# Performance work log

Hardware: AMD Instinct MI355X
Metric: run time of the kernel (lower is better)

## Reference

```python
import jax, jax.numpy as jnp
import numpy as np

REGION_DIM = 144
LLM_DIM = 3584
NUM_HEADS = 4
HEAD_DIM = REGION_DIM // NUM_HEADS          # 36
V_HEAD_DIM = LLM_DIM // NUM_HEADS           # 896
LN_EPS = 1e-5
N, M = 4096, 4096


def setup_inputs() -> dict:
    key = jax.random.key(0)
    ks = jax.random.split(key, 16)
    s = 0.02
    return {
        "target_emb": jax.random.normal(ks[0], (N, REGION_DIM), jnp.float32),
        "source_emb": jax.random.normal(ks[1], (M, LLM_DIM), jnp.float32),
        "value_emb":  jax.random.normal(ks[2], (M, LLM_DIM), jnp.float32),
        # params stored [in, out] (transposed vs torch nn.Linear)
        "wq_w": jax.random.normal(ks[3], (REGION_DIM, REGION_DIM), jnp.float32) * s,
        "wq_b": jnp.zeros((REGION_DIM,), jnp.float32),
        "wk_w": jax.random.normal(ks[4], (LLM_DIM, REGION_DIM), jnp.float32) * s,
        "wk_b": jnp.zeros((REGION_DIM,), jnp.float32),
        # per-head V projections stacked: [H, llm_dim, llm_dim//H]
        "wv_w": jax.random.normal(ks[5], (NUM_HEADS, LLM_DIM, V_HEAD_DIM), jnp.float32) * s,
        "wv_b": jnp.zeros((NUM_HEADS, V_HEAD_DIM), jnp.float32),
        "resid_w": jax.random.normal(ks[6], (REGION_DIM, LLM_DIM), jnp.float32) * s,
        "resid_b": jnp.zeros((LLM_DIM,), jnp.float32),
        "out_w": jax.random.normal(ks[7], (LLM_DIM, LLM_DIM), jnp.float32) * s,
        "out_b": jnp.zeros((LLM_DIM,), jnp.float32),
        "ln_g": jnp.ones((LLM_DIM,), jnp.float32),
        "ln_b": jnp.zeros((LLM_DIM,), jnp.float32),
    }


def reference(target_emb, source_emb, value_emb,
              wq_w, wq_b, wk_w, wk_b, wv_w, wv_b,
              resid_w, resid_b, out_w, out_b, ln_g, ln_b):
    n = target_emb.shape[0]
    # Q: [N, region_dim] -> [H, N, head_dim]; K: [M, llm_dim] -> [H, M, head_dim]
    Q = (target_emb @ wq_w + wq_b).reshape(n, NUM_HEADS, HEAD_DIM).transpose(1, 0, 2)
    K = (source_emb @ wk_w + wk_b).reshape(-1, NUM_HEADS, HEAD_DIM).transpose(1, 0, 2)
    scores = jnp.einsum('hnd,hmd->hnm', Q, K) / jnp.sqrt(jnp.float32(HEAD_DIM))
    attn = jax.nn.softmax(scores, axis=-1)      # dropout = identity (eval mode)
    # per-head value projections: [H, M, llm_dim//H]
    V = jnp.einsum('me,hed->hmd', value_emb, wv_w) + wv_b[:, None, :]
    ctx = jnp.einsum('hnm,hmd->nhd', attn, V).reshape(n, LLM_DIM)
    x = ctx + (target_emb @ resid_w + resid_b)   # residual_proj (region_dim != llm_dim)
    mu = jnp.mean(x, axis=-1, keepdims=True)
    var = jnp.mean(jnp.square(x - mu), axis=-1, keepdims=True)
    x = (x - mu) * jax.lax.rsqrt(var + LN_EPS) * ln_g + ln_b
    return x @ out_w + out_b
```

## Files before the change

### kernel.cpp

```cpp
#include <hip/hip_runtime.h>

typedef _Float16 f16;
typedef _Float16 f16x8 __attribute__((ext_vector_type(8)));
typedef float f32x4 __attribute__((ext_vector_type(4)));

#define REGION_DIM 144
#define LLM_DIM 3584
#define NUM_HEADS 4
#define HEAD_DIM 36
#define HEAD_PAD 64
#define QK_COLS 256
#define KPAD_REGION 160
#define V_HEAD 896
#define LN_EPS 1e-5f

__device__ __forceinline__ void gl_lds16(const f16* g, f16* l)
{
    __builtin_amdgcn_global_load_lds(
        (const __attribute__((address_space(1))) unsigned int*)g,
        (__attribute__((address_space(3))) unsigned int*)l, 16, 0, 0);
}

__global__ void k_convert_pad(const float* __restrict__ in, f16* __restrict__ out,
                              int Cin, int Cout)
{
    int r = blockIdx.y;
    int c = blockIdx.x * 256 + threadIdx.x;
    if (c >= Cout) return;
    float v = (c < Cin) ? in[(long)r * Cin + c] : 0.f;
    out[(long)r * Cout + c] = (f16)v;
}

__global__ void k_transpose(const float* __restrict__ in, f16* __restrict__ out,
                            int R, int C, int Rpad, int Cpad,
                            long in_bstride, long out_bstride)
{
    __shared__ float tile[32][33];
    const float* ip = in + (long)blockIdx.z * in_bstride;
    f16* op = out + (long)blockIdx.z * out_bstride;
    int r0 = blockIdx.y * 32, c0 = blockIdx.x * 32;
    int tx = threadIdx.x, ty = threadIdx.y;
#pragma unroll
    for (int i = 0; i < 32; i += 8) {
        int r = r0 + ty + i, c = c0 + tx;
        tile[ty + i][tx] = (r < R && c < C) ? ip[(long)r * C + c] : 0.f;
    }
    __syncthreads();
#pragma unroll
    for (int i = 0; i < 32; i += 8) {
        int c = c0 + ty + i, r = r0 + tx;
        if (c < Cpad && r < Rpad) op[(long)c * Rpad + r] = (f16)tile[tx][ty + i];
    }
}

__global__ void k_headpad_w(const float* __restrict__ w, const float* __restrict__ b,
                            f16* __restrict__ outW, float* __restrict__ outB,
                            int E, int Epad)
{
    int hp = blockIdx.y;
    int h = hp >> 6, kk = hp & 63;
    int d = h * HEAD_DIM + kk;
    bool valid = (kk < HEAD_DIM);
    int e = blockIdx.x * 256 + threadIdx.x;
    if (e < Epad) {
        float v = (valid && e < E) ? w[(long)e * REGION_DIM + d] : 0.f;
        outW[(long)hp * Epad + e] = (f16)v;
    }
    if (blockIdx.x == 0 && threadIdx.x == 0) outB[hp] = valid ? b[d] : 0.f;
}

enum { EPI_F16_EXPSCALE = 0,
       EPI_F16_BIASROW  = 1,
       EPI_F16_DIVROW   = 2,
       EPI_F32_BIASCOL  = 3,
       EPI_F16_BIASCOL  = 4 };

template <int EPI>
__global__ __launch_bounds__(256, 2)
void gemm_f16(const f16* __restrict__ A, int lda, long sAz,
              const f16* __restrict__ Bt, int ldb, long sBz,
              void* __restrict__ Cv, int ldc, long sCz,
              const float* __restrict__ bias, long sbz, float scale, int K)
{
    __shared__ __align__(16) f16 sA[128 * 32];
    __shared__ __align__(16) f16 sB[128 * 32];
    const int tid = threadIdx.x;
    const int z = blockIdx.z;
    A += (long)z * sAz;
    Bt += (long)z * sBz;
    if (bias) bias += (long)z * sbz;

    const int gx = gridDim.x, gy = gridDim.y;
    int pid = blockIdx.y * gx + blockIdx.x;
    const int GROUP = 8;
    int span = GROUP * gx;
    int gid = pid / span;
    int y0 = gid * GROUP;
    int gsz = (gy - y0 < GROUP) ? (gy - y0) : GROUP;
    int rem = pid - gid * span;
    const int by = y0 + rem % gsz;
    const int bx = rem / gsz;
    const int m0 = by * 128, n0 = bx * 128;

    const int w = tid >> 6, l = tid & 63;
    const int wu = __builtin_amdgcn_readfirstlane(w);
    const int wr = w >> 1, wc = w & 1;

    f32x4 acc[4][4] = {};

    const int srow = tid >> 2;
    const int scol = (tid & 3) * 8;
    const f16* Ag = A + (long)(m0 + srow) * lda + scol;
    const f16* Bg = Bt + (long)(n0 + srow) * ldb + scol;
    f16* sA0 = sA + wu * 512;
    f16* sA1 = sA + 2048 + wu * 512;
    f16* sB0 = sB + wu * 512;
    f16* sB1 = sB + 2048 + wu * 512;
    const int qk = (l >> 4) * 8;
    const int fr = l & 15;

    for (int k0 = 0; k0 < K; k0 += 32) {
        __syncthreads();
        gl_lds16(Ag + k0, sA0);
        gl_lds16(Ag + (long)64 * lda + k0, sA1);
        gl_lds16(Bg + k0, sB0);
        gl_lds16(Bg + (long)64 * ldb + k0, sB1);
        __syncthreads();

        f16x8 af[4], bf[4];
#pragma unroll
        for (int mt = 0; mt < 4; mt++)
            af[mt] = *(const f16x8*)&sA[(wr * 64 + mt * 16 + fr) * 32 + qk];
#pragma unroll
        for (int nt = 0; nt < 4; nt++)
            bf[nt] = *(const f16x8*)&sB[(wc * 64 + nt * 16 + fr) * 32 + qk];
#pragma unroll
        for (int mt = 0; mt < 4; mt++)
#pragma unroll
            for (int nt = 0; nt < 4; nt++)
                acc[mt][nt] = __builtin_amdgcn_mfma_f32_16x16x32_f16(af[mt], bf[nt], acc[mt][nt], 0, 0, 0);
    }

    const int q4 = (l >> 4) * 4;
    float bc[4];
#pragma unroll
    for (int nt = 0; nt < 4; nt++) {
        if constexpr (EPI == EPI_F16_BIASCOL || EPI == EPI_F32_BIASCOL)
            bc[nt] = bias[n0 + wc * 64 + nt * 16 + fr];
        else
            bc[nt] = 0.f;
    }
#pragma unroll
    for (int mt = 0; mt < 4; mt++)
#pragma unroll
        for (int r = 0; r < 4; r++) {
            int row = m0 + wr * 64 + mt * 16 + q4 + r;
            float rowv = 0.f;
            if constexpr (EPI == EPI_F16_BIASROW) rowv = bias[row];
            if constexpr (EPI == EPI_F16_DIVROW) rowv = 1.f / bias[row];
#pragma unroll
            for (int nt = 0; nt < 4; nt++) {
                int col = n0 + wc * 64 + nt * 16 + fr;
                float v = acc[mt][nt][r];
                if constexpr (EPI == EPI_F16_EXPSCALE) {
                    ((f16*)Cv + (long)z * sCz)[(long)row * ldc + col] = (f16)__expf(v * scale);
                } else if constexpr (EPI == EPI_F16_BIASROW) {
                    ((f16*)Cv + (long)z * sCz)[(long)row * ldc + col] = (f16)(v + rowv);
                } else if constexpr (EPI == EPI_F16_DIVROW) {
                    ((f16*)Cv + (long)z * sCz)[(long)row * ldc + col] = (f16)(v * rowv);
                } else if constexpr (EPI == EPI_F16_BIASCOL) {
                    ((f16*)Cv + (long)z * sCz)[(long)row * ldc + col] = (f16)(v + bc[nt]);
                } else {
                    ((float*)Cv + (long)z * sCz)[(long)row * ldc + col] = v + bc[nt];
                }
            }
        }
}

__global__ void k_rowsum(const f16* __restrict__ P, float* __restrict__ lsum,
                         long hstride)
{
    const f16x8* p8 = (const f16x8*)(P + (long)blockIdx.y * hstride + (long)blockIdx.x * 4096);
    int t = threadIdx.x, w = t >> 6, l = t & 63;
    f16x8 a = p8[t], b = p8[256 + t];
    float s = 0.f;
#pragma unroll
    for (int j = 0; j < 8; j++) s += (float)a[j] + (float)b[j];
#pragma unroll
    for (int o = 32; o; o >>= 1) s += __shfl_xor(s, o);
    __shared__ float red[4];
    if (l == 0) red[w] = s;
    __syncthreads();
    if (t == 0)
        lsum[(long)blockIdx.y * gridDim.x + blockIdx.x] = red[0] + red[1] + red[2] + red[3];
}

__global__ void k_layernorm(const f16* __restrict__ ctxp, const f16* __restrict__ resp,
                            const float* __restrict__ g, const float* __restrict__ be,
                            f16* __restrict__ out)
{
    long base = (long)blockIdx.x * LLM_DIM;
    const f16x8* c8 = (const f16x8*)(ctxp + base);
    const f16x8* r8 = (const f16x8*)(resp + base);
    int t = threadIdx.x, w = t >> 6, l = t & 63;
    bool has2 = t < 192;
    f16x8 a0 = c8[t], b0 = r8[t];
    f16x8 a1 = {}, b1 = {};
    if (has2) { a1 = c8[256 + t]; b1 = r8[256 + t]; }
    float v[16];
    float s = 0.f;
#pragma unroll
    for (int j = 0; j < 8; j++) { v[j] = (float)a0[j] + (float)b0[j]; s += v[j]; }
#pragma unroll
    for (int j = 0; j < 8; j++) v[8 + j] = (float)a1[j] + (float)b1[j];
    if (has2)
#pragma unroll
        for (int j = 0; j < 8; j++) s += v[8 + j];
#pragma unroll
    for (int o = 32; o; o >>= 1) s += __shfl_xor(s, o);
    __shared__ float r1[4];
    if (l == 0) r1[w] = s;
    __syncthreads();
    float mu = (r1[0] + r1[1] + r1[2] + r1[3]) * (1.f / LLM_DIM);
    float s2 = 0.f;
#pragma unroll
    for (int j = 0; j < 8; j++) { float d = v[j] - mu; s2 += d * d; }
    if (has2)
#pragma unroll
        for (int j = 8; j < 16; j++) { float d = v[j] - mu; s2 += d * d; }
#pragma unroll
    for (int o = 32; o; o >>= 1) s2 += __shfl_xor(s2, o);
    __shared__ float r2[4];
    if (l == 0) r2[w] = s2;
    __syncthreads();
    float var = (r2[0] + r2[1] + r2[2] + r2[3]) * (1.f / LLM_DIM);
    float inv = rsqrtf(var + LN_EPS);
    f16* op = out + base;
    f16x8 o0, o1;
#pragma unroll
    for (int j = 0; j < 8; j++) {
        int c = t * 8 + j;
        o0[j] = (f16)((v[j] - mu) * inv * g[c] + be[c]);
    }
    ((f16x8*)op)[t] = o0;
    if (has2) {
#pragma unroll
        for (int j = 0; j < 8; j++) {
            int c = (256 + t) * 8 + j;
            o1[j] = (f16)((v[8 + j] - mu) * inv * g[c] + be[c]);
        }
        ((f16x8*)op)[256 + t] = o1;
    }
}

extern "C" void kernel_launch(void* const* d_in, const int* in_sizes, int n_in,
                              void* d_out, int out_size, void* d_ws, size_t ws_size,
                              hipStream_t stream)
{
    const float* target  = (const float*)d_in[0];
    const float* source  = (const float*)d_in[1];
    const float* value   = (const float*)d_in[2];
    const float* wq_w    = (const float*)d_in[3];
    const float* wq_b    = (const float*)d_in[4];
    const float* wk_w    = (const float*)d_in[5];
    const float* wk_b    = (const float*)d_in[6];
    const float* wv_w    = (const float*)d_in[7];
    const float* wv_b    = (const float*)d_in[8];
    const float* resid_w = (const float*)d_in[9];
    const float* resid_b = (const float*)d_in[10];
    const float* out_w   = (const float*)d_in[11];
    const float* out_b   = (const float*)d_in[12];
    const float* ln_g    = (const float*)d_in[13];
    const float* ln_b    = (const float*)d_in[14];

    const int N = in_sizes[0] / REGION_DIM;
    const int M = in_sizes[1] / LLM_DIM;

    char* ws = (char*)d_ws;
    size_t off = 0;
    auto alloc = [&](size_t bytes) { void* p = ws + off; off += (bytes + 255) & ~(size_t)255; return p; };
    f16*   tgt16   = (f16*)alloc((size_t)N * KPAD_REGION * 2);
    f16*   residT  = (f16*)alloc((size_t)LLM_DIM * KPAD_REGION * 2);
    f16*   outT    = (f16*)alloc((size_t)LLM_DIM * LLM_DIM * 2);
    f16*   wqT     = (f16*)alloc((size_t)QK_COLS * KPAD_REGION * 2);
    float* biasK   = (float*)alloc(QK_COLS * 4);
    float* biasQ   = (float*)alloc(QK_COLS * 4);
    f16*   Qtmp    = (f16*)alloc((size_t)N * QK_COLS * 2);
    f16*   Ktmp    = (f16*)alloc((size_t)M * QK_COLS * 2);
    f16*   Vt      = (f16*)alloc((size_t)LLM_DIM * M * 2);
    f16*   residbf = (f16*)alloc((size_t)N * LLM_DIM * 2);
    f16*   ctx     = (f16*)alloc((size_t)N * LLM_DIM * 2);
    f16*   xln     = (f16*)alloc((size_t)N * LLM_DIM * 2);
    float* lsum    = (float*)alloc((size_t)2 * N * 4);
    const int HB = 2;
    char* U = (char*)alloc((size_t)HB * N * M * 2);
    f16* val16 = (f16*)U;
    f16* wvT   = (f16*)(U + (size_t)M * LLM_DIM * 2);
    f16* src16 = (f16*)U;
    f16* wkT   = (f16*)(U + (size_t)M * LLM_DIM * 2);
    f16* attnB = (f16*)U;
    (void)n_in; (void)out_size; (void)ws_size;

    dim3 tb(32, 8);

    k_convert_pad<<<dim3(1, N), 256, 0, stream>>>(target, tgt16, REGION_DIM, KPAD_REGION);
    k_transpose<<<dim3(LLM_DIM / 32, KPAD_REGION / 32, 1), tb, 0, stream>>>(
        resid_w, residT, REGION_DIM, LLM_DIM, KPAD_REGION, LLM_DIM, 0, 0);
    k_transpose<<<dim3(LLM_DIM / 32, LLM_DIM / 32, 1), tb, 0, stream>>>(
        out_w, outT, LLM_DIM, LLM_DIM, LLM_DIM, LLM_DIM, 0, 0);
    k_headpad_w<<<dim3(1, QK_COLS), 256, 0, stream>>>(wq_w, wq_b, wqT, biasQ, REGION_DIM, KPAD_REGION);

    gemm_f16<EPI_F16_BIASCOL><<<dim3(QK_COLS / 128, N / 128), 256, 0, stream>>>(
        tgt16, KPAD_REGION, 0, wqT, KPAD_REGION, 0, Qtmp, QK_COLS, 0, biasQ, 0, 1.f, KPAD_REGION);
    gemm_f16<EPI_F16_BIASCOL><<<dim3(LLM_DIM / 128, N / 128), 256, 0, stream>>>(
        tgt16, KPAD_REGION, 0, residT, KPAD_REGION, 0, residbf, LLM_DIM, 0, resid_b, 0, 1.f, KPAD_REGION);

    k_convert_pad<<<dim3(LLM_DIM / 256, M), 256, 0, stream>>>(value, val16, LLM_DIM, LLM_DIM);
    k_transpose<<<dim3(V_HEAD / 32, LLM_DIM / 32, NUM_HEADS), tb, 0, stream>>>(
        wv_w, wvT, LLM_DIM, V_HEAD, LLM_DIM, V_HEAD, (long)LLM_DIM * V_HEAD, (long)V_HEAD * LLM_DIM);
    gemm_f16<EPI_F16_BIASROW><<<dim3(M / 128, LLM_DIM / 128), 256, 0, stream>>>(
        wvT, LLM_DIM, 0, val16, LLM_DIM, 0, Vt, M, 0, wv_b, 0, 1.f, LLM_DIM);

    k_convert_pad<<<dim3(LLM_DIM / 256, M), 256, 0, stream>>>(source, src16, LLM_DIM, LLM_DIM);
    k_headpad_w<<<dim3(LLM_DIM / 256, QK_COLS), 256, 0, stream>>>(wk_w, wk_b, wkT, biasK, LLM_DIM, LLM_DIM);
    gemm_f16<EPI_F16_BIASCOL><<<dim3(QK_COLS / 128, M / 128), 256, 0, stream>>>(
        src16, LLM_DIM, 0, wkT, LLM_DIM, 0, Ktmp, QK_COLS, 0, biasK, 0, 1.f, LLM_DIM);

    const float sc = 0.16666667f;
    for (int h0 = 0; h0 < NUM_HEADS; h0 += HB) {
        gemm_f16<EPI_F16_EXPSCALE><<<dim3(M / 128, N / 128, HB), 256, 0, stream>>>(
            Qtmp + h0 * HEAD_PAD, QK_COLS, HEAD_PAD,
            Ktmp + h0 * HEAD_PAD, QK_COLS, HEAD_PAD,
            attnB, M, (long)N * M, nullptr, 0, sc, HEAD_PAD);
        k_rowsum<<<dim3(N, HB), 256, 0, stream>>>(attnB, lsum, (long)N * M);
        gemm_f16<EPI_F16_DIVROW><<<dim3(V_HEAD / 128, N / 128, HB), 256, 0, stream>>>(
            attnB, M, (long)N * M,
            Vt + (size_t)h0 * V_HEAD * M, M, (long)V_HEAD * M,
            ctx + (size_t)h0 * V_HEAD, LLM_DIM, V_HEAD, lsum, N, 1.f, M);
    }

    k_layernorm<<<N, 256, 0, stream>>>(ctx, residbf, ln_g, ln_b, xln);
    gemm_f16<EPI_F32_BIASCOL><<<dim3(LLM_DIM / 128, N / 128), 256, 0, stream>>>(
        xln, LLM_DIM, 0, outT, LLM_DIM, 0, (float*)d_out, LLM_DIM, 0, out_b, 0, 1.f, LLM_DIM);
}
```

Measured before the change: 931.9 us.

## Add 256x256-tile pipelined GEMM for V projection and output projection

Adds a new 512-thread GEMM kernel with 256x256 output tiles, double-buffered LDS fed by direct global-to-LDS loads, XCD-aware block swizzling, and interleaved sub-tile load/MFMA phases with priority raising. It is used for the two large K=3584 GEMMs (value projection and final output projection) in place of the 128x128 kernel. The aim is more data reuse per tile and better overlap of loads with MFMA work. In exchange it uses 128KB of LDS per block, fewer blocks, and many barriers per iteration.

```diff
diff --git a/kernel.cpp b/kernel.cpp
--- a/kernel.cpp
+++ b/kernel.cpp
@@ -20,6 +20,10 @@
         (const __attribute__((address_space(1))) unsigned int*)g,
         (__attribute__((address_space(3))) unsigned int*)l, 16, 0, 0);
 }
+
+#define S_BARRIER() do { asm volatile("" ::: "memory"); __builtin_amdgcn_s_barrier(); asm volatile("" ::: "memory"); } while (0)
+#define WAIT_LGKM0() asm volatile("s_waitcnt lgkmcnt(0)" ::: "memory")
+#define SCHED_FENCE() __builtin_amdgcn_sched_barrier(0)
 
 __global__ void k_convert_pad(const float* __restrict__ in, f16* __restrict__ out,
                               int Cin, int Cout)
@@ -172,6 +176,201 @@
                     ((f16*)Cv + (long)z * sCz)[(long)row * ldc + col] = (f16)(v + bc[nt]);
                 } else {
                     ((float*)Cv + (long)z * sCz)[(long)row * ldc + col] = v + bc[nt];
+                }
+            }
+        }
+}
+
+template <int EPI>
+__global__ __launch_bounds__(512, 2)
+void gemm256_f16(const f16* __restrict__ A, int lda,
+                 const f16* __restrict__ Bt, int ldb,
+                 void* __restrict__ Cv, int ldc,
+                 const float* __restrict__ bias, int K)
+{
+    __shared__ __align__(16) f16 sm[65536];
+    f16* smf = sm;
+
+    const int tid = threadIdx.x;
+    const int l = tid & 63;
+
+    const int gx = gridDim.x, gy = gridDim.y;
+    int pid = blockIdx.y * gx + blockIdx.x;
+    int nwg = gx * gy;
+    int q = nwg >> 3, r8 = nwg & 7;
+    int xcd = pid & 7, idx = pid >> 3;
+    int swz = (xcd < r8) ? (xcd * (q + 1) + idx)
+                         : (r8 * (q + 1) + (xcd - r8) * q + idx);
+    const int by = swz % gy, bx = swz / gy;
+    const int m0 = by * 256, n0 = bx * 256;
+
+    const int wu = __builtin_amdgcn_readfirstlane(tid >> 6);
+    const int wr = wu >> 2;
+    const int wc = wu & 3;
+    const int wst = wu * 512;
+
+    const int strow = wu * 8 + (l >> 3);
+    const int stcol = ((l & 7) ^ (l >> 3)) * 8;
+    const f16* Asrc = A + (size_t)(m0 + strow) * lda + stcol;
+    const f16* Bsrc = Bt + (size_t)(n0 + strow) * ldb + stcol;
+
+    const int fr = l & 15;
+    const int hi8 = (l >> 4) * 8;
+    const int swl = (fr & 7) * 8;
+    const int ca0 = hi8 ^ swl;
+    const int ca1 = (32 + hi8) ^ swl;
+
+    const int NT = K >> 6;
+
+    f32x4 acc[8][4] = {};
+    f16x8 af[4][2], bf0[2][2], bf1[2][2];
+
+    gl_lds16(Asrc, smf + wst);
+    gl_lds16(Asrc + (size_t)64 * lda, smf + 4096 + wst);
+    gl_lds16(Bsrc, smf + 16384 + wst);
+    gl_lds16(Bsrc + (size_t)64 * ldb, smf + 16384 + 4096 + wst);
+    gl_lds16(Asrc + (size_t)128 * lda, smf + 8192 + wst);
+    gl_lds16(Asrc + (size_t)192 * lda, smf + 8192 + 4096 + wst);
+    gl_lds16(Bsrc + (size_t)128 * ldb, smf + 16384 + 8192 + wst);
+    gl_lds16(Bsrc + (size_t)192 * ldb, smf + 16384 + 8192 + 4096 + wst);
+    if (NT > 1) {
+        gl_lds16(Bsrc + 64, smf + 32768 + 16384 + wst);
+        gl_lds16(Bsrc + 64 + (size_t)64 * ldb, smf + 32768 + 16384 + 4096 + wst);
+        gl_lds16(Asrc + 64, smf + 32768 + wst);
+        gl_lds16(Asrc + 64 + (size_t)64 * lda, smf + 32768 + 4096 + wst);
+        asm volatile("s_waitcnt vmcnt(4)" ::: "memory");
+    } else {
+        asm volatile("s_waitcnt vmcnt(0)" ::: "memory");
+    }
+    S_BARRIER();
+
+#define MFMA16(MB, NB, BF)                                                            \
+    _Pragma("unroll") for (int i = 0; i < 4; i++)                                     \
+    _Pragma("unroll") for (int j = 0; j < 2; j++) {                                   \
+        acc[MB + i][NB + j] = __builtin_amdgcn_mfma_f32_16x16x32_f16(                 \
+            af[i][0], BF[j][0], acc[MB + i][NB + j], 0, 0, 0);                        \
+        acc[MB + i][NB + j] = __builtin_amdgcn_mfma_f32_16x16x32_f16(                 \
+            af[i][1], BF[j][1], acc[MB + i][NB + j], 0, 0, 0);                        \
+    }
+
+    for (int t = 0; t < NT; ++t) {
+        const int p = t & 1;
+        const f16* sAp = smf + (p << 15) + wr * 8192 + fr * 64;
+        const f16* sBp = smf + (p << 15) + 16384 + wc * 4096 + fr * 64;
+
+#pragma unroll
+        for (int i = 0; i < 4; i++) {
+            af[i][0] = *(const f16x8*)(sAp + i * 1024 + ca0);
+            af[i][1] = *(const f16x8*)(sAp + i * 1024 + ca1);
+        }
+#pragma unroll
+        for (int j = 0; j < 2; j++) {
+            bf0[j][0] = *(const f16x8*)(sBp + j * 1024 + ca0);
+            bf0[j][1] = *(const f16x8*)(sBp + j * 1024 + ca1);
+        }
+        if (t + 1 < NT) {
+            const f16* s = Asrc + (size_t)128 * lda + (size_t)(t + 1) * 64;
+            f16* d = smf + ((p ^ 1) << 15) + 8192 + wst;
+            gl_lds16(s, d);
+            gl_lds16(s + (size_t)64 * lda, d + 4096);
+        }
+        S_BARRIER();
+        WAIT_LGKM0();
+        SCHED_FENCE();
+        __builtin_amdgcn_s_setprio(1);
+        MFMA16(0, 0, bf0);
+        __builtin_amdgcn_s_setprio(0);
+        WAIT_LGKM0();
+        S_BARRIER();
+
+#pragma unroll
+        for (int j = 0; j < 2; j++) {
+            bf1[j][0] = *(const f16x8*)(sBp + 2048 + j * 1024 + ca0);
+            bf1[j][1] = *(const f16x8*)(sBp + 2048 + j * 1024 + ca1);
+        }
+        if (t + 1 < NT) {
+            const f16* s = Bsrc + (size_t)128 * ldb + (size_t)(t + 1) * 64;
+            f16* d = smf + ((p ^ 1) << 15) + 16384 + 8192 + wst;
+            gl_lds16(s, d);
+            gl_lds16(s + (size_t)64 * ldb, d + 4096);
+        }
+        S_BARRIER();
+        WAIT_LGKM0();
+        SCHED_FENCE();
+        __builtin_amdgcn_s_setprio(1);
+        MFMA16(0, 2, bf1);
+        __builtin_amdgcn_s_setprio(0);
+        WAIT_LGKM0();
+        S_BARRIER();
+
+#pragma unroll
+        for (int i = 0; i < 4; i++) {
+            af[i][0] = *(const f16x8*)(sAp + 4096 + i * 1024 + ca0);
+            af[i][1] = *(const f16x8*)(sAp + 4096 + i * 1024 + ca1);
+        }
+        if (t + 2 < NT) {
+            const f16* s = Bsrc + (size_t)(t + 2) * 64;
+            f16* d = smf + (p << 15) + 16384 + wst;
+            gl_lds16(s, d);
+            gl_lds16(s + (size_t)64 * ldb, d + 4096);
+        }
+        S_BARRIER();
+        WAIT_LGKM0();
+        SCHED_FENCE();
+        __builtin_amdgcn_s_setprio(1);
+        MFMA16(4, 2, bf1);
+        __builtin_amdgcn_s_setprio(0);
+        WAIT_LGKM0();
+        S_BARRIER();
+
+        if (t + 2 < NT) {
+            const f16* s = Asrc + (size_t)(t + 2) * 64;
+            f16* d = smf + (p << 15) + wst;
+            gl_lds16(s, d);
+            gl_lds16(s + (size_t)64 * lda, d + 4096);
+        }
+        S_BARRIER();
+        __builtin_amdgcn_s_setprio(1);
+        MFMA16(4, 0, bf0);
+        __builtin_amdgcn_s_setprio(0);
+        if (t + 2 < NT) {
+            asm volatile("s_waitcnt vmcnt(4)" ::: "memory");
+        } else if (t + 1 < NT) {
+            asm volatile("s_waitcnt vmcnt(0)" ::: "memory");
+        }
+        S_BARRIER();
+    }
+#undef MFMA16
+
+    const int q4 = (l >> 4) * 4;
+    float bc[4];
+#pragma unroll
+    for (int nt = 0; nt < 4; nt++) {
+        if constexpr (EPI == EPI_F16_BIASCOL || EPI == EPI_F32_BIASCOL)
+            bc[nt] = bias[n0 + wc * 64 + nt * 16 + fr];
+        else
+            bc[nt] = 0.f;
+    }
+#pragma unroll
+    for (int mt = 0; mt < 8; mt++)
+#pragma unroll
+        for (int r = 0; r < 4; r++) {
+            int row = m0 + wr * 128 + mt * 16 + q4 + r;
+            float rowv = 0.f;
+            if constexpr (EPI == EPI_F16_BIASROW) rowv = bias[row];
+            if constexpr (EPI == EPI_F16_DIVROW) rowv = 1.f / bias[row];
+#pragma unroll
+            for (int nt = 0; nt < 4; nt++) {
+                int col = n0 + wc * 64 + nt * 16 + fr;
+                float v = acc[mt][nt][r];
+                if constexpr (EPI == EPI_F16_BIASROW) {
+                    ((f16*)Cv)[(size_t)row * ldc + col] = (f16)(v + rowv);
+                } else if constexpr (EPI == EPI_F16_DIVROW) {
+                    ((f16*)Cv)[(size_t)row * ldc + col] = (f16)(v * rowv);
+                } else if constexpr (EPI == EPI_F16_BIASCOL) {
+                    ((f16*)Cv)[(size_t)row * ldc + col] = (f16)(v + bc[nt]);
+                } else {
+                    ((float*)Cv)[(size_t)row * ldc + col] = v + bc[nt];
                 }
             }
         }
@@ -318,8 +517,8 @@
     k_convert_pad<<<dim3(LLM_DIM / 256, M), 256, 0, stream>>>(value, val16, LLM_DIM, LLM_DIM);
     k_transpose<<<dim3(V_HEAD / 32, LLM_DIM / 32, NUM_HEADS), tb, 0, stream>>>(
         wv_w, wvT, LLM_DIM, V_HEAD, LLM_DIM, V_HEAD, (long)LLM_DIM * V_HEAD, (long)V_HEAD * LLM_DIM);
-    gemm_f16<EPI_F16_BIASROW><<<dim3(M / 128, LLM_DIM / 128), 256, 0, stream>>>(
-        wvT, LLM_DIM, 0, val16, LLM_DIM, 0, Vt, M, 0, wv_b, 0, 1.f, LLM_DIM);
+    gemm256_f16<EPI_F16_BIASROW><<<dim3(M / 256, LLM_DIM / 256), 512, 0, stream>>>(
+        wvT, LLM_DIM, val16, LLM_DIM, Vt, M, wv_b, LLM_DIM);
 
     k_convert_pad<<<dim3(LLM_DIM / 256, M), 256, 0, stream>>>(source, src16, LLM_DIM, LLM_DIM);
     k_headpad_w<<<dim3(LLM_DIM / 256, QK_COLS), 256, 0, stream>>>(wk_w, wk_b, wkT, biasK, LLM_DIM, LLM_DIM);
@@ -340,6 +539,6 @@
     }
 
     k_layernorm<<<N, 256, 0, stream>>>(ctx, residbf, ln_g, ln_b, xln);
-    gemm_f16<EPI_F32_BIASCOL><<<dim3(LLM_DIM / 128, N / 128), 256, 0, stream>>>(
-        xln, LLM_DIM, 0, outT, LLM_DIM, 0, (float*)d_out, LLM_DIM, 0, out_b, 0, 1.f, LLM_DIM);
-}
+    gemm256_f16<EPI_F32_BIASCOL><<<dim3(LLM_DIM / 256, N / 256), 512, 0, stream>>>(
+        xln, LLM_DIM, outT, LLM_DIM, (float*)d_out, LLM_DIM, out_b, LLM_DIM);
+}
```

After: 845.6 us. -9.3%, faster.
